# Kernel optimization log

Hardware: AMD Instinct MI355X
Metric: run time of the kernel (lower is better)

## Reference

```python
import jax, jax.numpy as jnp
import numpy as np

N = 50000        # nodes
E = 800000       # edges (avg degree 16)
DIN = 256        # input feature dim
D = 128          # embedding_dim
B = 8            # graphs in batch
ITERS = 2        # num_iterations


def setup_inputs() -> dict:
    key = jax.random.key(0)
    ks = jax.random.split(key, 16)
    w = lambda k, shape: jax.random.normal(k, shape, jnp.float32) * 0.05
    z = lambda n: jnp.zeros((n,), jnp.float32)
    return {
        "nodes": jax.random.normal(ks[0], (N, DIN), jnp.float32),
        "edges": jax.random.randint(ks[1], (2, E), 0, N),
        "batch": jnp.sort(jax.random.randint(ks[2], (N,), 0, B)),
        # initial encoder Linear(DIN, D)
        "W_enc": w(ks[3], (DIN, D)), "b_enc": z(D),
        # parent aggregation MLP: Linear(2D, D) -> ReLU -> Linear(D, D)
        "Wp1": w(ks[4], (2 * D, D)), "bp1": z(D),
        "Wp2": w(ks[5], (D, D)), "bp2": z(D),
        # child aggregation MLP
        "Wc1": w(ks[6], (2 * D, D)), "bc1": z(D),
        "Wc2": w(ks[7], (D, D)), "bc2": z(D),
        # final agg: Linear(3D, 2D) -> ReLU -> Linear(2D, D)
        "Wf1": w(ks[8], (3 * D, 2 * D)), "bf1": z(2 * D),
        "Wf2": w(ks[9], (2 * D, D)), "bf2": z(D),
        # Conv1d(D, 2D, kernel=1) == Linear(D, 2D)
        "Wconv": w(ks[10], (D, 2 * D)), "bconv": z(2 * D),
    }


def _edge_agg(x, idx_i, idx_j, W1, b1, W2, b2, inv_deg):
    # message: mlp(cat(x_i, x_j)); scatter-sum at idx_i; degree-normalize.
    h = jnp.concatenate([x[idx_i], x[idx_j]], axis=1)         # [E, 2D]
    m = jax.nn.relu(h @ W1 + b1) @ W2 + b2                    # [E, D]
    agg = jax.ops.segment_sum(m, idx_i, num_segments=x.shape[0])
    return agg * inv_deg[:, None]


def reference(nodes, edges, batch, W_enc, b_enc, Wp1, bp1, Wp2, bp2,
              Wc1, bc1, Wc2, bc2, Wf1, bf1, Wf2, bf2, Wconv, bconv):
    src, dst = edges[0], edges[1]
    ones_e = jnp.ones((edges.shape[1],), nodes.dtype)
    deg_dst = jax.ops.segment_sum(ones_e, dst, num_segments=N)
    deg_src = jax.ops.segment_sum(ones_e, src, num_segments=N)
    inv_dst = jnp.where(deg_dst > 0, 1.0 / deg_dst, 0.0)
    inv_src = jnp.where(deg_src > 0, 1.0 / deg_src, 0.0)

    x = nodes @ W_enc + b_enc                                  # [N, D]
    for _ in range(ITERS):
        # Parent_Aggregation: x_i = x[dst], x_j = x[src], sum at dst, / in-deg
        fi = _edge_agg(x, dst, src, Wp1, bp1, Wp2, bp2, inv_dst)
        # Child_Aggregation:  x_i = x[src], x_j = x[dst], sum at src, / out-deg
        fo = _edge_agg(x, src, dst, Wc1, bc1, Wc2, bc2, inv_src)
        h = jnp.concatenate([x, fi, fo], axis=1)               # [N, 3D]
        x = x + (jax.nn.relu(h @ Wf1 + bf1) @ Wf2 + bf2)

    y = x @ Wconv + bconv                                      # conv1d k=1 -> [N, 2D]
    gmax = jax.ops.segment_max(y, batch, num_segments=B)       # global_max_pool
    cnt = jax.ops.segment_sum(jnp.ones((N,), y.dtype), batch, num_segments=B)
    gmean = jax.ops.segment_sum(y, batch, num_segments=B) / cnt[:, None]
    return jnp.concatenate([gmax, gmean], axis=1)              # [B, 4D]
```

## Files before the change

### kernel.cpp

```cpp
#include <hip/hip_runtime.h>
#include <hip/hip_bf16.h>
#include <float.h>

typedef __hip_bfloat16 bf16;
typedef short short8 __attribute__((ext_vector_type(8)));
typedef short short4v __attribute__((ext_vector_type(4)));
typedef float f32x4 __attribute__((ext_vector_type(4)));

__device__ __forceinline__ float toF(bf16 v) { return __bfloat162float(v); }
__device__ __forceinline__ float s2f(short s) {
    return __uint_as_float(((unsigned int)(unsigned short)s) << 16);
}
__device__ __forceinline__ short f2s(float f) {
    bf16 h = __float2bfloat16(f);
    return *(short*)&h;
}

__global__ void diag_kernel(float* __restrict__ out, float v, int n) {
    int i = blockIdx.x * 256 + threadIdx.x;
    if (i < n) out[i] = v;
}

__global__ void init_kernel(int* __restrict__ deg2, float* __restrict__ cnt_gsum,
                            float* __restrict__ gmax, int* __restrict__ flag, int n2) {
    int i = blockIdx.x * 256 + threadIdx.x;
    if (i < n2) deg2[i] = 0;
    if (i < 8 + 2048) cnt_gsum[i] = 0.f;
    if (i < 2048) gmax[i] = -FLT_MAX;
    if (i == 0) *flag = 1;
}

__global__ void probe_kernel(const unsigned int* __restrict__ w, int nwords,
                             int* __restrict__ flag) {
    int i = blockIdx.x * 256 + threadIdx.x;
    bool bad = false;
    if (i < nwords) {
        float v = __uint_as_float((w[i] & 0xFFFFu) << 16);
        bad = !(v > -1e3f && v < 1e3f);
    }
    if (__any(bad) && (threadIdx.x & 63) == 0) atomicAnd(flag, 0);
}

struct M1 {
    const int* edges; int E; int CAP;
    int* degd; int* degs; int* adjd; int* adjs;
    const void* nsrc; bf16* ndst; int nElems;
    const void* bsrc[8]; bf16* bdst[8]; int bn[8];
    const void* wsrc[10]; int woff[10]; bf16* wdst[10];
    int wK[10]; int wNC[10]; int wstart[11];
    const int* batch; int Nn; float* cnt;
    const int* flag;
    int sCnt, sSwz, sBias, sConv;
};

__global__ void mega1_kernel(M1 a) {
    int b = blockIdx.x, tid = threadIdx.x;
    if (b < a.sCnt) {
        const int* es = a.edges;
        const int* ed = a.edges + a.E;
        int e0 = (b * 256 + tid) * 4;
        if (e0 + 4 <= a.E) {
            int4 s4 = *(const int4*)(es + e0);
            int4 d4 = *(const int4*)(ed + e0);
            int sl;
            sl = atomicAdd(&a.degs[s4.x], 1); a.adjs[s4.x * a.CAP + sl] = d4.x;
            sl = atomicAdd(&a.degs[s4.y], 1); a.adjs[s4.y * a.CAP + sl] = d4.y;
            sl = atomicAdd(&a.degs[s4.z], 1); a.adjs[s4.z * a.CAP + sl] = d4.z;
            sl = atomicAdd(&a.degs[s4.w], 1); a.adjs[s4.w * a.CAP + sl] = d4.w;
            sl = atomicAdd(&a.degd[d4.x], 1); a.adjd[d4.x * a.CAP + sl] = s4.x;
            sl = atomicAdd(&a.degd[d4.y], 1); a.adjd[d4.y * a.CAP + sl] = s4.y;
            sl = atomicAdd(&a.degd[d4.z], 1); a.adjd[d4.z * a.CAP + sl] = s4.z;
            sl = atomicAdd(&a.degd[d4.w], 1); a.adjd[d4.w * a.CAP + sl] = s4.w;
        } else {
            for (int e = e0; e < a.E; ++e) {
                int s_ = es[e], d_ = ed[e];
                int sl = atomicAdd(&a.degs[s_], 1); a.adjs[s_ * a.CAP + sl] = d_;
                sl     = atomicAdd(&a.degd[d_], 1); a.adjd[d_ * a.CAP + sl] = s_;
            }
        }
    } else if (b < a.sSwz) {
        __shared__ float loc[8];
        if (tid < 8) loc[tid] = 0.f;
        __syncthreads();
        int i = (b - a.sCnt) * 256 + tid;
        if (i < a.Nn) atomicAdd(&loc[a.batch[i]], 1.0f);
        __syncthreads();
        if (tid < 8 && loc[tid] > 0.f) atomicAdd(&a.cnt[tid], loc[tid]);
    } else if (b < a.sBias) {
        int bb = b - a.sSwz;
        int seg = 0;
#pragma unroll
        for (int t = 1; t < 10; ++t) if (bb >= a.wstart[t]) seg = t;
        int i = (bb - a.wstart[seg]) * 256 + tid;
        int K = a.wK[seg], NC = a.wNC[seg];
        if (i < K * NC) {
            int KF = K >> 5;
            int j = i & 7;
            int ln = (i >> 3) & 63;
            int q = i >> 9;
            int kb = q % KF;
            int t = q / KF;
            int k = kb * 32 + (ln >> 4) * 8 + j;
            int n = t * 16 + (ln & 15);
            int idx = a.woff[seg] + k * NC + n;
            a.wdst[seg][i] = (*a.flag)
                ? ((const bf16*)a.wsrc[seg])[idx]
                : __float2bfloat16(((const float*)a.wsrc[seg])[idx]);
        }
    } else if (b < a.sConv) {
#pragma unroll
        for (int t = 0; t < 8; ++t)
            for (int i = tid; i < a.bn[t]; i += 256)
                a.bdst[t][i] = (*a.flag)
                    ? ((const bf16*)a.bsrc[t])[i]
                    : __float2bfloat16(((const float*)a.bsrc[t])[i]);
    } else {
        if (*a.flag) return;
        int i = (b - a.sConv) * 2048 + tid * 8;
        if (i + 8 <= a.nElems) {
            const float* f = (const float*)a.nsrc + i;
            short8 o;
#pragma unroll
            for (int j = 0; j < 8; ++j) o[j] = f2s(f[j]);
            *(short8*)((short*)a.ndst + i) = o;
        } else {
            int e = a.nElems;
            for (int jj = i; jj < e && jj < i + 8; ++jj)
                a.ndst[jj] = __float2bfloat16(((const float*)a.nsrc)[jj]);
        }
    }
}

__device__ __forceinline__ void atomicMaxF(float* addr, float val) {
    unsigned int* ua = (unsigned int*)addr;
    unsigned int old = __float_as_uint(*addr);
    while (__uint_as_float(old) < val) {
        unsigned int assumed = old;
        old = atomicCAS(ua, assumed, __float_as_uint(val));
        if (old == assumed) break;
    }
}

template<int K, int NC> struct SB {
    static constexpr int APAD = K + 8;
    static constexpr int CPAD = NC + 8;
    static constexpr int AB = 64 * APAD * 2;
    static constexpr int CB = 64 * CPAD * 2;
    static constexpr int S = AB > CB ? AB : CB;
};

template<int K, int NC, int NSRC, bool RELU, bool RES, bool SCALE, bool POOL, bool STORE>
__device__ __forceinline__ void gemm_core(int bx,
    const bf16* A0, const bf16* A1, const bf16* A2,
    const bf16* WS, const bf16* bias, const float* scale, bf16* C, int M,
    const int* batch, float* gmax, float* gsum, char* smem) {
    constexpr int KF = K / 32;
    constexpr int NH = NC / 128;
    constexpr int APAD = SB<K, NC>::APAD;
    constexpr int CPAD = SB<K, NC>::CPAD;
    short* sA = (short*)smem;

    int tid = threadIdx.x;
    int m0blk = bx * 64;

    constexpr int C8 = K / 8;
    for (int idx = tid; idx < 64 * C8; idx += 256) {
        int r = idx / C8, c8 = idx % C8;
        int row = m0blk + r; row = row < M ? row : M - 1;
        const bf16* src;
        int off;
        if (NSRC == 1) { src = A0; off = c8 * 8; }
        else {
            int seg = c8 >> 4;
            src = seg == 0 ? A0 : (seg == 1 ? A1 : A2);
            off = (c8 & 15) * 8;
        }
        const size_t rs = (NSRC == 1) ? (size_t)K : (size_t)128;
        *(short8*)(sA + r * APAD + c8 * 8) = *(const short8*)((const short*)src + (size_t)row * rs + off);
    }
    __syncthreads();

    int wv = tid >> 6, ln = tid & 63;
    int quad = ln >> 4, ncol = ln & 15;
    int mw = wv * 16;

    short8 a[KF];
#pragma unroll
    for (int kb = 0; kb < KF; ++kb)
        a[kb] = *(const short8*)(sA + (mw + ncol) * APAD + kb * 32 + quad * 8);
    __syncthreads();

    float scl[4];
    if (SCALE) {
#pragma unroll
        for (int r = 0; r < 4; ++r) {
            int orow = m0blk + mw + quad * 4 + r;
            scl[r] = scale[orow < M ? orow : M - 1];
        }
    }

    short* sC = (short*)smem;
    const short8* wsp = (const short8*)WS;
#pragma unroll
    for (int h = 0; h < NH; ++h) {
        f32x4 acc[8];
#pragma unroll
        for (int t = 0; t < 8; ++t) acc[t] = (f32x4){0.f, 0.f, 0.f, 0.f};
        short8 bcur[8], bnxt[8];
#pragma unroll
        for (int t = 0; t < 8; ++t)
            bcur[t] = wsp[(size_t)((h * 8 + t) * KF) * 64 + ln];
#pragma unroll
        for (int kb = 0; kb < KF; ++kb) {
            if (kb + 1 < KF) {
#pragma unroll
                for (int t = 0; t < 8; ++t)
                    bnxt[t] = wsp[(size_t)((h * 8 + t) * KF + kb + 1) * 64 + ln];
            }
#pragma unroll
            for (int t = 0; t < 8; ++t)
                acc[t] = __builtin_amdgcn_mfma_f32_16x16x32_bf16(a[kb], bcur[t], acc[t], 0, 0, 0);
#pragma unroll
            for (int t = 0; t < 8; ++t) bcur[t] = bnxt[t];
        }
#pragma unroll
        for (int t = 0; t < 8; ++t) {
            float bv = bias ? toF(bias[h * 128 + t * 16 + ncol]) : 0.f;
#pragma unroll
            for (int r = 0; r < 4; ++r) {
                float v = acc[t][r];
                if (SCALE) { v *= scl[r]; if (scl[r] > 0.f) v += bv; }
                else v += bv;
                if (RELU) v = fmaxf(v, 0.f);
                sC[(mw + quad * 4 + r) * CPAD + h * 128 + t * 16 + ncol] = f2s(v);
            }
        }
    }
    __syncthreads();
    if (!STORE && !POOL) return;

    if (POOL) {
        int* bs = (int*)(smem + SB<K, NC>::S);
        if (tid < 64) {
            int row = m0blk + tid;
            bs[tid] = (row < M) ? batch[row] : -1;
        }
        __syncthreads();
        int cur_b = -1;
        float mx = -FLT_MAX, sm = 0.f;
        for (int r = 0; r < 64; ++r) {
            int b = bs[r];
            if (b < 0) break;
            float v = s2f(sC[r * CPAD + tid]);
            if (b != cur_b) {
                if (cur_b >= 0) {
                    atomicMaxF(&gmax[cur_b * 256 + tid], mx);
                    atomicAdd(&gsum[cur_b * 256 + tid], sm);
                }
                cur_b = b; mx = v; sm = v;
            } else {
                mx = fmaxf(mx, v);
                sm += v;
            }
        }
        if (cur_b >= 0) {
            atomicMaxF(&gmax[cur_b * 256 + tid], mx);
            atomicAdd(&gsum[cur_b * 256 + tid], sm);
        }
    } else {
        constexpr int OC8 = NC / 8;
        for (int idx = tid; idx < 64 * OC8; idx += 256) {
            int r = idx / OC8, c8 = idx % OC8;
            int row = m0blk + r;
            if (row < M) {
                short8 v = *(short8*)(sC + r * CPAD + c8 * 8);
                size_t o = (size_t)row * NC + c8 * 8;
                if (RES) {
                    short8 old = *(const short8*)((const short*)C + o);
#pragma unroll
                    for (int j = 0; j < 8; ++j) v[j] = f2s(s2f(v[j]) + s2f(old[j]));
                }
                *(short8*)((short*)C + o) = v;
            }
        }
    }
}

template<int K, int NC, int NSRC, bool RELU, bool RES, bool SCALE, bool POOL>
__global__ __launch_bounds__(256, 2)
void gemm_mfma_kernel(const bf16* A0, const bf16* A1, const bf16* A2,
                      const bf16* WS, const bf16* bias,
                      const float* scale, bf16* C, int M,
                      const int* batch, float* gmax, float* gsum) {
    __shared__ __align__(16) char smem[SB<K, NC>::S + (POOL ? 256 : 0)];
    gemm_core<K, NC, NSRC, RELU, RES, SCALE, POOL, true>(
        blockIdx.x, A0, A1, A2, WS, bias, scale, C, M, batch, gmax, gsum, smem);
}

__global__ __launch_bounds__(256, 2)
void enc_inv_kernel(const void* nodes_raw, const bf16* Tn, const int* flag,
                    const bf16* WSenc, const bf16* benc, bf16* x, int M, int gb,
                    const int* degd, const int* degs,
                    float* invd, float* invs) {
    __shared__ __align__(16) char smem[SB<256, 128>::S];
    if ((int)blockIdx.x < gb) {
        const bf16* A0 = (*flag) ? (const bf16*)nodes_raw : Tn;
        gemm_core<256, 128, 1, false, false, false, false, true>(
            blockIdx.x, A0, nullptr, nullptr, WSenc, benc, nullptr, x, M,
            nullptr, nullptr, nullptr, smem);
    } else {
        int i = ((int)blockIdx.x - gb) * 256 + threadIdx.x;
        if (i < M) {
            int dd = degd[i]; invd[i] = dd > 0 ? 1.0f / (float)dd : 0.0f;
            int ds = degs[i]; invs[i] = ds > 0 ? 1.0f / (float)ds : 0.0f;
        }
    }
}

__global__ __launch_bounds__(256, 2)
void gemm_dual_kernel(const bf16* Sp, const bf16* WS2, const bf16* b2,
                      const float* inv, bf16* Fi,
                      const bf16* x, const bf16* WSpq, bf16* T,
                      int M, int split) {
    __shared__ __align__(16) char smem[SB<128, 256>::S];
    if (blockIdx.x < split)
        gemm_core<128, 128, 1, false, false, true, false, true>(
            blockIdx.x, Sp, nullptr, nullptr, WS2, b2, inv, Fi, M, nullptr, nullptr, nullptr, smem);
    else
        gemm_core<128, 256, 1, false, false, false, false, true>(
            blockIdx.x - split, x, nullptr, nullptr, WSpq, nullptr, nullptr, T, M, nullptr, nullptr, nullptr, smem);
}

__global__ __launch_bounds__(256, 2)
void fused_mlp_kernel(const bf16* x, const bf16* Fi, const bf16* Fo,
                      const bf16* WSf1, const bf16* bf1_,
                      const bf16* WSf2, const bf16* bf2_,
                      bf16* xio, int M) {
    __shared__ __align__(16) char smem[SB<384, 256>::S];
    gemm_core<384, 256, 3, true, false, false, false, false>(
        blockIdx.x, x, Fi, Fo, WSf1, bf1_, nullptr, nullptr, M,
        nullptr, nullptr, nullptr, smem);

    constexpr int HPAD = 264;
    constexpr int CPAD2 = 136;
    short* sH = (short*)smem;
    int tid = threadIdx.x;
    int wv = tid >> 6, ln = tid & 63;
    int quad = ln >> 4, ncol = ln & 15;
    int mw = wv * 16;
    int m0blk = blockIdx.x * 64;

    short8 a2[8];
#pragma unroll
    for (int kb = 0; kb < 8; ++kb)
        a2[kb] = *(const short8*)(sH + (mw + ncol) * HPAD + kb * 32 + quad * 8);
    __syncthreads();

    f32x4 acc[8];
#pragma unroll
    for (int t = 0; t < 8; ++t) acc[t] = (f32x4){0.f, 0.f, 0.f, 0.f};
    const short8* wsp = (const short8*)WSf2;
    short8 bcur[8], bnxt[8];
#pragma unroll
    for (int t = 0; t < 8; ++t) bcur[t] = wsp[(size_t)(t * 8) * 64 + ln];
#pragma unroll
    for (int kb = 0; kb < 8; ++kb) {
        if (kb + 1 < 8) {
#pragma unroll
            for (int t = 0; t < 8; ++t)
                bnxt[t] = wsp[(size_t)(t * 8 + kb + 1) * 64 + ln];
        }
#pragma unroll
        for (int t = 0; t < 8; ++t)
            acc[t] = __builtin_amdgcn_mfma_f32_16x16x32_bf16(a2[kb], bcur[t], acc[t], 0, 0, 0);
#pragma unroll
        for (int t = 0; t < 8; ++t) bcur[t] = bnxt[t];
    }
    short* sC2 = (short*)smem;
#pragma unroll
    for (int t = 0; t < 8; ++t) {
        float bv = toF(bf2_[t * 16 + ncol]);
#pragma unroll
        for (int r = 0; r < 4; ++r)
            sC2[(mw + quad * 4 + r) * CPAD2 + t * 16 + ncol] = f2s(acc[t][r] + bv);
    }
    __syncthreads();
    for (int idx = tid; idx < 64 * 16; idx += 256) {
        int r = idx >> 4, c8 = idx & 15;
        int row = m0blk + r;
        if (row < M) {
            short8 v = *(short8*)(sC2 + r * CPAD2 + c8 * 8);
            size_t o = (size_t)row * 128 + c8 * 8;
            short8 old = *(const short8*)((const short*)xio + o);
#pragma unroll
            for (int j = 0; j < 8; ++j) v[j] = f2s(s2f(v[j]) + s2f(old[j]));
            *(short8*)((short*)xio + o) = v;
        }
    }
}

__global__ void agg_kernel(const int* __restrict__ deg, const int* __restrict__ adj, int CAP,
                           const bf16* __restrict__ PQ, const bf16* __restrict__ b1,
                           bf16* __restrict__ S, int M) {
    int tid = threadIdx.x;
    int wv = tid >> 6, ln = tid & 63;
    int node = blockIdx.x * 4 + wv;
    if (node >= M) return;
    int c4 = ln & 31, half = ln >> 5;
    float p[4];
    {
        short4v pv = *(const short4v*)((const short*)PQ + (size_t)node * 256 + 4 * c4);
        short4v bv = *(const short4v*)((const short*)b1 + 4 * c4);
#pragma unroll
        for (int r = 0; r < 4; ++r) p[r] = s2f(pv[r]) + s2f(bv[r]);
    }
    float a[4] = {0.f, 0.f, 0.f, 0.f};
    int beg = node * CAP;
    int end = beg + deg[node];
    const short* Qb = (const short*)PQ + 128 + 4 * c4;
    int k = beg + half;
    for (; k + 14 < end; k += 16) {
        int j0 = adj[k],      j1 = adj[k + 2],  j2 = adj[k + 4],  j3 = adj[k + 6];
        int j4 = adj[k + 8],  j5 = adj[k + 10], j6 = adj[k + 12], j7 = adj[k + 14];
        short4v q0 = *(const short4v*)(Qb + (size_t)j0 * 256);
        short4v q1 = *(const short4v*)(Qb + (size_t)j1 * 256);
        short4v q2 = *(const short4v*)(Qb + (size_t)j2 * 256);
        short4v q3 = *(const short4v*)(Qb + (size_t)j3 * 256);
        short4v q4 = *(const short4v*)(Qb + (size_t)j4 * 256);
        short4v q5 = *(const short4v*)(Qb + (size_t)j5 * 256);
        short4v q6 = *(const short4v*)(Qb + (size_t)j6 * 256);
        short4v q7 = *(const short4v*)(Qb + (size_t)j7 * 256);
#pragma unroll
        for (int r = 0; r < 4; ++r)
            a[r] += fmaxf(p[r] + s2f(q0[r]), 0.f) + fmaxf(p[r] + s2f(q1[r]), 0.f)
                  + fmaxf(p[r] + s2f(q2[r]), 0.f) + fmaxf(p[r] + s2f(q3[r]), 0.f)
                  + fmaxf(p[r] + s2f(q4[r]), 0.f) + fmaxf(p[r] + s2f(q5[r]), 0.f)
                  + fmaxf(p[r] + s2f(q6[r]), 0.f) + fmaxf(p[r] + s2f(q7[r]), 0.f);
    }
    for (; k + 6 < end; k += 8) {
        int j0 = adj[k], j1 = adj[k + 2], j2 = adj[k + 4], j3 = adj[k + 6];
        short4v q0 = *(const short4v*)(Qb + (size_t)j0 * 256);
        short4v q1 = *(const short4v*)(Qb + (size_t)j1 * 256);
        short4v q2 = *(const short4v*)(Qb + (size_t)j2 * 256);
        short4v q3 = *(const short4v*)(Qb + (size_t)j3 * 256);
#pragma unroll
        for (int r = 0; r < 4; ++r)
            a[r] += fmaxf(p[r] + s2f(q0[r]), 0.f) + fmaxf(p[r] + s2f(q1[r]), 0.f)
                  + fmaxf(p[r] + s2f(q2[r]), 0.f) + fmaxf(p[r] + s2f(q3[r]), 0.f);
    }
    for (; k < end; k += 2) {
        int j = adj[k];
        short4v q = *(const short4v*)(Qb + (size_t)j * 256);
#pragma unroll
        for (int r = 0; r < 4; ++r) a[r] += fmaxf(p[r] + s2f(q[r]), 0.f);
    }
#pragma unroll
    for (int r = 0; r < 4; ++r) a[r] += __shfl_xor(a[r], 32);
    if (half == 0) {
        short4v o;
#pragma unroll
        for (int r = 0; r < 4; ++r) o[r] = f2s(a[r]);
        *(short4v*)((short*)S + (size_t)node * 128 + 4 * c4) = o;
    }
}

__global__ void out_kernel(const float* __restrict__ gmax, const float* __restrict__ gsum,
                           const float* __restrict__ cnt, const int* __restrict__ flag,
                           void* __restrict__ out) {
    int i = blockIdx.x * 256 + threadIdx.x;
    if (i < 8 * 512) {
        int b = i >> 9, c = i & 511;
        float v = (c < 256) ? gmax[b * 256 + c] : gsum[b * 256 + (c - 256)] / cnt[b];
        int f = *flag;
        if (!(v == v)) v = 1000.f + 100.f * (float)f;
        if (f) ((bf16*)out)[i] = __float2bfloat16(v);
        else   ((float*)out)[i] = v;
    }
}

extern "C" void kernel_launch(void* const* d_in, const int* in_sizes, int n_in,
                              void* d_out, int out_size, void* d_ws, size_t ws_size,
                              hipStream_t stream) {
    const int* edges = (const int*)d_in[1];
    const int* batch = (const int*)d_in[2];

    const int N_ = in_sizes[2];
    const int E_ = in_sizes[1] / 2;
    const size_t ND = (size_t)N_ * 128;

    char* p = (char*)d_ws;
    bf16* x  = (bf16*)p;      p += ND * 2;
    bf16* T  = (bf16*)p;      p += (size_t)N_ * 256 * 2;
    bf16* S  = (bf16*)p;      p += ND * 2;
    bf16* Fi = (bf16*)p;      p += ND * 2;
    bf16* bias[8];
    for (int t = 0; t < 8; ++t) { bias[t] = (bf16*)p; p += 512 * 2; }
    bf16* WSenc  = (bf16*)p;  p += 256 * 128 * 2;
    bf16* WSpq_p = (bf16*)p;  p += 256 * 128 * 2;
    bf16* WSpq_c = (bf16*)p;  p += 256 * 128 * 2;
    bf16* WS2p   = (bf16*)p;  p += 128 * 128 * 2;
    bf16* WS2c   = (bf16*)p;  p += 128 * 128 * 2;
    bf16* WSf1   = (bf16*)p;  p += 384 * 256 * 2;
    bf16* WSf2   = (bf16*)p;  p += 256 * 128 * 2;
    bf16* WSconv = (bf16*)p;  p += 128 * 256 * 2;
    int* degd    = (int*)p;   p += (size_t)N_ * 4;
    int* degs    = (int*)p;   p += (size_t)N_ * 4;
    float* invd  = (float*)p; p += (size_t)N_ * 4;
    float* invs  = (float*)p; p += (size_t)N_ * 4;
    float* cnt   = (float*)p; p += 8 * 4;
    float* gsum  = (float*)p; p += 2048 * 4;
    float* gmax  = (float*)p; p += 2048 * 4;
    int* flag    = (int*)p;   p += 64;

    size_t used = (size_t)(p - (char*)d_ws);
    size_t rem = ws_size > used ? ws_size - used : 0;
    int CAP = 0;
    if (rem >= (size_t)2 * N_ * 64 * 4) CAP = 64;
    else if (rem >= (size_t)2 * N_ * 48 * 4) CAP = 48;
    if (!CAP) {
        diag_kernel<<<(out_size + 255) / 256, 256, 0, stream>>>((float*)d_out, (float)(ws_size >> 20), out_size);
        return;
    }
    int* adjd = (int*)p;      p += (size_t)N_ * CAP * 4;
    int* adjs = (int*)p;

    int gN  = (N_ + 255) / 256;
    int gE4 = (E_ + 1023) / 1024;
    int gb  = (N_ + 63) / 64;
    int ga  = (N_ + 3) / 4;

    init_kernel<<<(2 * N_ + 255) / 256, 256, 0, stream>>>(degd, cnt, gmax, flag, 2 * N_);
    probe_kernel<<<8, 256, 0, stream>>>((const unsigned int*)d_in[3], 2048, flag);

    M1 a;
    a.edges = edges; a.E = E_; a.CAP = CAP;
    a.degd = degd; a.degs = degs; a.adjd = adjd; a.adjs = adjs;
    a.nsrc = d_in[0]; a.ndst = T; a.nElems = in_sizes[0];
    {
        const int bidx[8] = {4, 6, 8, 10, 12, 14, 16, 18};
        for (int t = 0; t < 8; ++t) {
            a.bsrc[t] = d_in[bidx[t]];
            a.bdst[t] = bias[t];
            a.bn[t] = in_sizes[bidx[t]];
        }
        const void* wraw[10] = {d_in[3], d_in[5], d_in[5], d_in[9], d_in[9],
                                d_in[7], d_in[11], d_in[13], d_in[15], d_in[17]};
        int woff[10]  = {0, 0, 128 * 128, 0, 128 * 128, 0, 0, 0, 0, 0};
        bf16* wdst[10] = {WSenc, WSpq_p, WSpq_p + 128 * 128, WSpq_c, WSpq_c + 128 * 128,
                          WS2p, WS2c, WSf1, WSf2, WSconv};
        int wK[10]  = {256, 128, 128, 128, 128, 128, 128, 384, 256, 128};
        int wNC[10] = {128, 128, 128, 128, 128, 128, 128, 256, 128, 256};
        int wb_ = 0;
        for (int t = 0; t < 10; ++t) {
            a.wsrc[t] = wraw[t]; a.woff[t] = woff[t]; a.wdst[t] = wdst[t];
            a.wK[t] = wK[t]; a.wNC[t] = wNC[t];
            a.wstart[t] = wb_;
            wb_ += (wK[t] * wNC[t] + 255) / 256;
        }
        a.wstart[10] = wb_;
        a.batch = batch; a.Nn = N_; a.cnt = cnt; a.flag = flag;
        a.sCnt  = gE4;
        a.sSwz  = a.sCnt + gN;
        a.sBias = a.sSwz + wb_;
        a.sConv = a.sBias + 1;
        int convB = (a.nElems + 2047) / 2048;
        mega1_kernel<<<a.sConv + convB, 256, 0, stream>>>(a);
    }

    enc_inv_kernel<<<gb + gN, 256, 0, stream>>>(d_in[0], T, flag, WSenc, bias[0],
                                                x, N_, gb, degd, degs, invd, invs);

    for (int it = 0; it < 2; ++it) {
        gemm_mfma_kernel<128, 256, 1, false, false, false, false><<<gb, 256, 0, stream>>>(
            x, nullptr, nullptr, WSpq_p, nullptr, nullptr, T, N_, nullptr, nullptr, nullptr);
        agg_kernel<<<ga, 256, 0, stream>>>(degd, adjd, CAP, T, bias[1], S, N_);
        gemm_dual_kernel<<<2 * gb, 256, 0, stream>>>(S, WS2p, bias[2], invd, Fi,
                                                     x, WSpq_c, T, N_, gb);
        agg_kernel<<<ga, 256, 0, stream>>>(degs, adjs, CAP, T, bias[3], S, N_);
        gemm_mfma_kernel<128, 128, 1, false, false, true, false><<<gb, 256, 0, stream>>>(
            S, nullptr, nullptr, WS2c, bias[4], invs, S, N_, nullptr, nullptr, nullptr);
        fused_mlp_kernel<<<gb, 256, 0, stream>>>(x, Fi, S, WSf1, bias[5], WSf2, bias[6], x, N_);
    }

    gemm_mfma_kernel<128, 256, 1, false, false, false, true><<<gb, 256, 0, stream>>>(
        x, nullptr, nullptr, WSconv, bias[7], nullptr, nullptr, N_, batch, gmax, gsum);
    out_kernel<<<16, 256, 0, stream>>>(gmax, gsum, cnt, flag, d_out);
}
```

Measured before the change: 645.0 us.

## Fuse per-iteration MLPs and conv pooling, compact adjacency to u16 ranks

Edge adjacency construction is split into a rank-recording atomic pass followed by a scatter pass, and neighbour indices are stored as u16 to halve adjacency bandwidth. The parent and child projections are computed in one wide GEMM, and both aggregations run in a single launch. The second-layer GEMMs, final MLP and (on the last iteration) conv plus pooling are fused into one mega kernel, which cuts launches and round trips of intermediates through global memory. Rank is stored as u8 and N must be below 65536, which limits generality. The fused kernel uses more shared memory and registers, which may reduce occupancy.

```diff
diff --git a/kernel.cpp b/kernel.cpp
--- a/kernel.cpp
+++ b/kernel.cpp
@@ -6,6 +6,8 @@
 typedef short short8 __attribute__((ext_vector_type(8)));
 typedef short short4v __attribute__((ext_vector_type(4)));
 typedef float f32x4 __attribute__((ext_vector_type(4)));
+typedef unsigned short u16;
+typedef unsigned char u8;
 
 __device__ __forceinline__ float toF(bf16 v) { return __bfloat162float(v); }
 __device__ __forceinline__ float s2f(short s) {
@@ -42,13 +44,13 @@
 }
 
 struct M1 {
-    const int* edges; int E; int CAP;
-    int* degd; int* degs; int* adjd; int* adjs;
-    const void* nsrc; bf16* ndst; int nElems;
-    const void* bsrc[8]; bf16* bdst[8]; int bn[8];
+    const int* edges; int E;
+    int* degd; int* degs; u8* rankd; u8* ranks;
+    const int* batch; int Nn; float* cnt;
     const void* wsrc[10]; int woff[10]; bf16* wdst[10];
     int wK[10]; int wNC[10]; int wstart[11];
-    const int* batch; int Nn; float* cnt;
+    const void* bsrc[8]; bf16* bdst[8]; int bn[8];
+    const void* nsrc; bf16* ndst; int nElems;
     const int* flag;
     int sCnt, sSwz, sBias, sConv;
 };
@@ -62,20 +64,21 @@
         if (e0 + 4 <= a.E) {
             int4 s4 = *(const int4*)(es + e0);
             int4 d4 = *(const int4*)(ed + e0);
-            int sl;
-            sl = atomicAdd(&a.degs[s4.x], 1); a.adjs[s4.x * a.CAP + sl] = d4.x;
-            sl = atomicAdd(&a.degs[s4.y], 1); a.adjs[s4.y * a.CAP + sl] = d4.y;
-            sl = atomicAdd(&a.degs[s4.z], 1); a.adjs[s4.z * a.CAP + sl] = d4.z;
-            sl = atomicAdd(&a.degs[s4.w], 1); a.adjs[s4.w * a.CAP + sl] = d4.w;
-            sl = atomicAdd(&a.degd[d4.x], 1); a.adjd[d4.x * a.CAP + sl] = s4.x;
-            sl = atomicAdd(&a.degd[d4.y], 1); a.adjd[d4.y * a.CAP + sl] = s4.y;
-            sl = atomicAdd(&a.degd[d4.z], 1); a.adjd[d4.z * a.CAP + sl] = s4.z;
-            sl = atomicAdd(&a.degd[d4.w], 1); a.adjd[d4.w * a.CAP + sl] = s4.w;
+            uchar4 rs, rd;
+            rs.x = (u8)atomicAdd(&a.degs[s4.x], 1);
+            rs.y = (u8)atomicAdd(&a.degs[s4.y], 1);
+            rs.z = (u8)atomicAdd(&a.degs[s4.z], 1);
+            rs.w = (u8)atomicAdd(&a.degs[s4.w], 1);
+            rd.x = (u8)atomicAdd(&a.degd[d4.x], 1);
+            rd.y = (u8)atomicAdd(&a.degd[d4.y], 1);
+            rd.z = (u8)atomicAdd(&a.degd[d4.z], 1);
+            rd.w = (u8)atomicAdd(&a.degd[d4.w], 1);
+            *(uchar4*)(a.ranks + e0) = rs;
+            *(uchar4*)(a.rankd + e0) = rd;
         } else {
             for (int e = e0; e < a.E; ++e) {
-                int s_ = es[e], d_ = ed[e];
-                int sl = atomicAdd(&a.degs[s_], 1); a.adjs[s_ * a.CAP + sl] = d_;
-                sl     = atomicAdd(&a.degd[d_], 1); a.adjd[d_ * a.CAP + sl] = s_;
+                a.ranks[e] = (u8)atomicAdd(&a.degs[es[e]], 1);
+                a.rankd[e] = (u8)atomicAdd(&a.degd[ed[e]], 1);
             }
         }
     } else if (b < a.sSwz) {
@@ -298,18 +301,44 @@
 }
 
 __global__ __launch_bounds__(256, 2)
-void enc_inv_kernel(const void* nodes_raw, const bf16* Tn, const int* flag,
-                    const bf16* WSenc, const bf16* benc, bf16* x, int M, int gb,
-                    const int* degd, const int* degs,
-                    float* invd, float* invs) {
+void sei_kernel(const int* __restrict__ edges, int E,
+                const u8* __restrict__ rankd, const u8* __restrict__ ranks,
+                u16* __restrict__ adjd, u16* __restrict__ adjs, int CAP,
+                const void* nodes_raw, const bf16* Tn, const int* flag,
+                const bf16* WSenc, const bf16* benc, bf16* x, int M,
+                const int* degd, const int* degs,
+                float* invd, float* invs, int gsc, int gb) {
     __shared__ __align__(16) char smem[SB<256, 128>::S];
-    if ((int)blockIdx.x < gb) {
+    int b = blockIdx.x, tid = threadIdx.x;
+    if (b < gsc) {
+        int e0 = (b * 256 + tid) * 4;
+        if (e0 + 4 <= E) {
+            int4 s4 = *(const int4*)(edges + e0);
+            int4 d4 = *(const int4*)(edges + E + e0);
+            uchar4 rs = *(const uchar4*)(ranks + e0);
+            uchar4 rd = *(const uchar4*)(rankd + e0);
+            if (rs.x < CAP) adjs[s4.x * CAP + rs.x] = (u16)d4.x;
+            if (rs.y < CAP) adjs[s4.y * CAP + rs.y] = (u16)d4.y;
+            if (rs.z < CAP) adjs[s4.z * CAP + rs.z] = (u16)d4.z;
+            if (rs.w < CAP) adjs[s4.w * CAP + rs.w] = (u16)d4.w;
+            if (rd.x < CAP) adjd[d4.x * CAP + rd.x] = (u16)s4.x;
+            if (rd.y < CAP) adjd[d4.y * CAP + rd.y] = (u16)s4.y;
+            if (rd.z < CAP) adjd[d4.z * CAP + rd.z] = (u16)s4.z;
+            if (rd.w < CAP) adjd[d4.w * CAP + rd.w] = (u16)s4.w;
+        } else {
+            for (int e = e0; e < E; ++e) {
+                int s_ = edges[e], d_ = edges[E + e];
+                if (ranks[e] < CAP) adjs[s_ * CAP + ranks[e]] = (u16)d_;
+                if (rankd[e] < CAP) adjd[d_ * CAP + rankd[e]] = (u16)s_;
+            }
+        }
+    } else if (b < gsc + gb) {
         const bf16* A0 = (*flag) ? (const bf16*)nodes_raw : Tn;
         gemm_core<256, 128, 1, false, false, false, false, true>(
-            blockIdx.x, A0, nullptr, nullptr, WSenc, benc, nullptr, x, M,
+            b - gsc, A0, nullptr, nullptr, WSenc, benc, nullptr, x, M,
             nullptr, nullptr, nullptr, smem);
     } else {
-        int i = ((int)blockIdx.x - gb) * 256 + threadIdx.x;
+        int i = (b - gsc - gb) * 256 + tid;
         if (i < M) {
             int dd = degd[i]; invd[i] = dd > 0 ? 1.0f / (float)dd : 0.0f;
             int ds = degs[i]; invs[i] = ds > 0 ? 1.0f / (float)ds : 0.0f;
@@ -317,119 +346,35 @@
     }
 }
 
-__global__ __launch_bounds__(256, 2)
-void gemm_dual_kernel(const bf16* Sp, const bf16* WS2, const bf16* b2,
-                      const float* inv, bf16* Fi,
-                      const bf16* x, const bf16* WSpq, bf16* T,
-                      int M, int split) {
-    __shared__ __align__(16) char smem[SB<128, 256>::S];
-    if (blockIdx.x < split)
-        gemm_core<128, 128, 1, false, false, true, false, true>(
-            blockIdx.x, Sp, nullptr, nullptr, WS2, b2, inv, Fi, M, nullptr, nullptr, nullptr, smem);
-    else
-        gemm_core<128, 256, 1, false, false, false, false, true>(
-            blockIdx.x - split, x, nullptr, nullptr, WSpq, nullptr, nullptr, T, M, nullptr, nullptr, nullptr, smem);
-}
-
-__global__ __launch_bounds__(256, 2)
-void fused_mlp_kernel(const bf16* x, const bf16* Fi, const bf16* Fo,
-                      const bf16* WSf1, const bf16* bf1_,
-                      const bf16* WSf2, const bf16* bf2_,
-                      bf16* xio, int M) {
-    __shared__ __align__(16) char smem[SB<384, 256>::S];
-    gemm_core<384, 256, 3, true, false, false, false, false>(
-        blockIdx.x, x, Fi, Fo, WSf1, bf1_, nullptr, nullptr, M,
-        nullptr, nullptr, nullptr, smem);
-
-    constexpr int HPAD = 264;
-    constexpr int CPAD2 = 136;
-    short* sH = (short*)smem;
-    int tid = threadIdx.x;
-    int wv = tid >> 6, ln = tid & 63;
-    int quad = ln >> 4, ncol = ln & 15;
-    int mw = wv * 16;
-    int m0blk = blockIdx.x * 64;
-
-    short8 a2[8];
-#pragma unroll
-    for (int kb = 0; kb < 8; ++kb)
-        a2[kb] = *(const short8*)(sH + (mw + ncol) * HPAD + kb * 32 + quad * 8);
-    __syncthreads();
-
-    f32x4 acc[8];
-#pragma unroll
-    for (int t = 0; t < 8; ++t) acc[t] = (f32x4){0.f, 0.f, 0.f, 0.f};
-    const short8* wsp = (const short8*)WSf2;
-    short8 bcur[8], bnxt[8];
-#pragma unroll
-    for (int t = 0; t < 8; ++t) bcur[t] = wsp[(size_t)(t * 8) * 64 + ln];
-#pragma unroll
-    for (int kb = 0; kb < 8; ++kb) {
-        if (kb + 1 < 8) {
-#pragma unroll
-            for (int t = 0; t < 8; ++t)
-                bnxt[t] = wsp[(size_t)(t * 8 + kb + 1) * 64 + ln];
-        }
-#pragma unroll
-        for (int t = 0; t < 8; ++t)
-            acc[t] = __builtin_amdgcn_mfma_f32_16x16x32_bf16(a2[kb], bcur[t], acc[t], 0, 0, 0);
-#pragma unroll
-        for (int t = 0; t < 8; ++t) bcur[t] = bnxt[t];
-    }
-    short* sC2 = (short*)smem;
-#pragma unroll
-    for (int t = 0; t < 8; ++t) {
-        float bv = toF(bf2_[t * 16 + ncol]);
-#pragma unroll
-        for (int r = 0; r < 4; ++r)
-            sC2[(mw + quad * 4 + r) * CPAD2 + t * 16 + ncol] = f2s(acc[t][r] + bv);
-    }
-    __syncthreads();
-    for (int idx = tid; idx < 64 * 16; idx += 256) {
-        int r = idx >> 4, c8 = idx & 15;
-        int row = m0blk + r;
-        if (row < M) {
-            short8 v = *(short8*)(sC2 + r * CPAD2 + c8 * 8);
-            size_t o = (size_t)row * 128 + c8 * 8;
-            short8 old = *(const short8*)((const short*)xio + o);
-#pragma unroll
-            for (int j = 0; j < 8; ++j) v[j] = f2s(s2f(v[j]) + s2f(old[j]));
-            *(short8*)((short*)xio + o) = v;
-        }
-    }
-}
-
-__global__ void agg_kernel(const int* __restrict__ deg, const int* __restrict__ adj, int CAP,
-                           const bf16* __restrict__ PQ, const bf16* __restrict__ b1,
-                           bf16* __restrict__ S, int M) {
-    int tid = threadIdx.x;
-    int wv = tid >> 6, ln = tid & 63;
-    int node = blockIdx.x * 4 + wv;
-    if (node >= M) return;
+__device__ __forceinline__ void agg_body(int node, int tid,
+        const int* __restrict__ deg, const u16* __restrict__ adj, int CAP,
+        const short* __restrict__ PQ, int stride,
+        const short* __restrict__ b1, bf16* __restrict__ S) {
+    int ln = tid & 63;
     int c4 = ln & 31, half = ln >> 5;
     float p[4];
     {
-        short4v pv = *(const short4v*)((const short*)PQ + (size_t)node * 256 + 4 * c4);
-        short4v bv = *(const short4v*)((const short*)b1 + 4 * c4);
+        short4v pv = *(const short4v*)(PQ + (size_t)node * stride + 4 * c4);
+        short4v bv = *(const short4v*)(b1 + 4 * c4);
 #pragma unroll
         for (int r = 0; r < 4; ++r) p[r] = s2f(pv[r]) + s2f(bv[r]);
     }
     float a[4] = {0.f, 0.f, 0.f, 0.f};
-    int beg = node * CAP;
-    int end = beg + deg[node];
-    const short* Qb = (const short*)PQ + 128 + 4 * c4;
-    int k = beg + half;
-    for (; k + 14 < end; k += 16) {
-        int j0 = adj[k],      j1 = adj[k + 2],  j2 = adj[k + 4],  j3 = adj[k + 6];
-        int j4 = adj[k + 8],  j5 = adj[k + 10], j6 = adj[k + 12], j7 = adj[k + 14];
-        short4v q0 = *(const short4v*)(Qb + (size_t)j0 * 256);
-        short4v q1 = *(const short4v*)(Qb + (size_t)j1 * 256);
-        short4v q2 = *(const short4v*)(Qb + (size_t)j2 * 256);
-        short4v q3 = *(const short4v*)(Qb + (size_t)j3 * 256);
-        short4v q4 = *(const short4v*)(Qb + (size_t)j4 * 256);
-        short4v q5 = *(const short4v*)(Qb + (size_t)j5 * 256);
-        short4v q6 = *(const short4v*)(Qb + (size_t)j6 * 256);
-        short4v q7 = *(const short4v*)(Qb + (size_t)j7 * 256);
+    int d = deg[node]; d = d < CAP ? d : CAP;
+    const u16* ap = adj + (size_t)node * CAP;
+    const short* Qb = PQ + 128 + 4 * c4;
+    int k = half;
+    for (; k + 14 < d; k += 16) {
+        int j0 = ap[k],      j1 = ap[k + 2],  j2 = ap[k + 4],  j3 = ap[k + 6];
+        int j4 = ap[k + 8],  j5 = ap[k + 10], j6 = ap[k + 12], j7 = ap[k + 14];
+        short4v q0 = *(const short4v*)(Qb + (size_t)j0 * stride);
+        short4v q1 = *(const short4v*)(Qb + (size_t)j1 * stride);
+        short4v q2 = *(const short4v*)(Qb + (size_t)j2 * stride);
+        short4v q3 = *(const short4v*)(Qb + (size_t)j3 * stride);
+        short4v q4 = *(const short4v*)(Qb + (size_t)j4 * stride);
+        short4v q5 = *(const short4v*)(Qb + (size_t)j5 * stride);
+        short4v q6 = *(const short4v*)(Qb + (size_t)j6 * stride);
+        short4v q7 = *(const short4v*)(Qb + (size_t)j7 * stride);
 #pragma unroll
         for (int r = 0; r < 4; ++r)
             a[r] += fmaxf(p[r] + s2f(q0[r]), 0.f) + fmaxf(p[r] + s2f(q1[r]), 0.f)
@@ -437,20 +382,20 @@
                   + fmaxf(p[r] + s2f(q4[r]), 0.f) + fmaxf(p[r] + s2f(q5[r]), 0.f)
                   + fmaxf(p[r] + s2f(q6[r]), 0.f) + fmaxf(p[r] + s2f(q7[r]), 0.f);
     }
-    for (; k + 6 < end; k += 8) {
-        int j0 = adj[k], j1 = adj[k + 2], j2 = adj[k + 4], j3 = adj[k + 6];
-        short4v q0 = *(const short4v*)(Qb + (size_t)j0 * 256);
-        short4v q1 = *(const short4v*)(Qb + (size_t)j1 * 256);
-        short4v q2 = *(const short4v*)(Qb + (size_t)j2 * 256);
-        short4v q3 = *(const short4v*)(Qb + (size_t)j3 * 256);
+    for (; k + 6 < d; k += 8) {
+        int j0 = ap[k], j1 = ap[k + 2], j2 = ap[k + 4], j3 = ap[k + 6];
+        short4v q0 = *(const short4v*)(Qb + (size_t)j0 * stride);
+        short4v q1 = *(const short4v*)(Qb + (size_t)j1 * stride);
+        short4v q2 = *(const short4v*)(Qb + (size_t)j2 * stride);
+        short4v q3 = *(const short4v*)(Qb + (size_t)j3 * stride);
 #pragma unroll
         for (int r = 0; r < 4; ++r)
             a[r] += fmaxf(p[r] + s2f(q0[r]), 0.f) + fmaxf(p[r] + s2f(q1[r]), 0.f)
                   + fmaxf(p[r] + s2f(q2[r]), 0.f) + fmaxf(p[r] + s2f(q3[r]), 0.f);
     }
-    for (; k < end; k += 2) {
-        int j = adj[k];
-        short4v q = *(const short4v*)(Qb + (size_t)j * 256);
+    for (; k < d; k += 2) {
+        int j = ap[k];
+        short4v q = *(const short4v*)(Qb + (size_t)j * stride);
 #pragma unroll
         for (int r = 0; r < 4; ++r) a[r] += fmaxf(p[r] + s2f(q[r]), 0.f);
     }
@@ -461,6 +406,233 @@
 #pragma unroll
         for (int r = 0; r < 4; ++r) o[r] = f2s(a[r]);
         *(short4v*)((short*)S + (size_t)node * 128 + 4 * c4) = o;
+    }
+}
+
+__global__ void agg_kernel(const int* deg, const u16* adj, int CAP,
+                           const bf16* PQ, int stride, const bf16* b1,
+                           bf16* S, int M) {
+    int node = blockIdx.x * 4 + (threadIdx.x >> 6);
+    if (node >= M) return;
+    agg_body(node, threadIdx.x, deg, adj, CAP, (const short*)PQ, stride,
+             (const short*)b1, S);
+}
+
+__global__ void agg2_kernel(const int* degd, const u16* adjd,
+                            const int* degs, const u16* adjs, int CAP,
+                            const bf16* T, const bf16* b1p, const bf16* b1c,
+                            bf16* Sd, bf16* Ss, int M, int ga) {
+    int b = blockIdx.x, wv = threadIdx.x >> 6;
+    if (b < ga) {
+        int node = b * 4 + wv;
+        if (node < M)
+            agg_body(node, threadIdx.x, degd, adjd, CAP, (const short*)T, 512,
+                     (const short*)b1p, Sd);
+    } else {
+        int node = (b - ga) * 4 + wv;
+        if (node < M)
+            agg_body(node, threadIdx.x, degs, adjs, CAP, (const short*)T + 256, 512,
+                     (const short*)b1c, Ss);
+    }
+}
+
+template<bool FINAL>
+__global__ __launch_bounds__(256, 2)
+void mega_mlp_kernel(const bf16* __restrict__ x, const bf16* Sd, const bf16* Ss,
+                     const bf16* WS2p, const bf16* b2p, const float* invd,
+                     const bf16* WS2c, const bf16* b2c, const float* invs,
+                     const bf16* WSf1, const bf16* bf1_,
+                     const bf16* WSf2, const bf16* bf2_,
+                     bf16* xio, int M,
+                     const bf16* WSconv, const bf16* bconv,
+                     const int* batch, float* gmax, float* gsum) {
+    __shared__ __align__(16) char smem[52224 + 256];
+    constexpr int RB = 17408;
+    short* sm = (short*)smem;
+    int tid = threadIdx.x;
+    int m0blk = blockIdx.x * 64;
+
+    for (int idx = tid; idx < 64 * 16; idx += 256) {
+        int r = idx >> 4, c8 = idx & 15;
+        int row = m0blk + r; row = row < M ? row : M - 1;
+        *(short8*)(sm + r * 136 + c8 * 8) =
+            *(const short8*)((const short*)x + (size_t)row * 128 + c8 * 8);
+    }
+    gemm_core<128, 128, 1, false, false, true, false, false>(
+        blockIdx.x, Sd, nullptr, nullptr, WS2p, b2p, invd, nullptr, M,
+        nullptr, nullptr, nullptr, smem + RB);
+    gemm_core<128, 128, 1, false, false, true, false, false>(
+        blockIdx.x, Ss, nullptr, nullptr, WS2c, b2c, invs, nullptr, M,
+        nullptr, nullptr, nullptr, smem + 2 * RB);
+
+    int wv = tid >> 6, ln = tid & 63;
+    int quad = ln >> 4, ncol = ln & 15;
+    int mw = wv * 16;
+
+    short8 a1[12];
+#pragma unroll
+    for (int kb = 0; kb < 12; ++kb) {
+        const short* sb = sm + (kb >> 2) * (RB / 2);
+        a1[kb] = *(const short8*)(sb + (mw + ncol) * 136 + (kb & 3) * 32 + quad * 8);
+    }
+    __syncthreads();
+
+    short* sH = sm + RB / 2;
+    const short8* w1 = (const short8*)WSf1;
+#pragma unroll
+    for (int h = 0; h < 2; ++h) {
+        f32x4 acc[8];
+#pragma unroll
+        for (int t = 0; t < 8; ++t) acc[t] = (f32x4){0.f, 0.f, 0.f, 0.f};
+        short8 bcur[8], bnxt[8];
+#pragma unroll
+        for (int t = 0; t < 8; ++t)
+            bcur[t] = w1[(size_t)((h * 8 + t) * 12) * 64 + ln];
+#pragma unroll
+        for (int kb = 0; kb < 12; ++kb) {
+            if (kb + 1 < 12) {
+#pragma unroll
+                for (int t = 0; t < 8; ++t)
+                    bnxt[t] = w1[(size_t)((h * 8 + t) * 12 + kb + 1) * 64 + ln];
+            }
+#pragma unroll
+            for (int t = 0; t < 8; ++t)
+                acc[t] = __builtin_amdgcn_mfma_f32_16x16x32_bf16(a1[kb], bcur[t], acc[t], 0, 0, 0);
+#pragma unroll
+            for (int t = 0; t < 8; ++t) bcur[t] = bnxt[t];
+        }
+#pragma unroll
+        for (int t = 0; t < 8; ++t) {
+            float bv = toF(bf1_[h * 128 + t * 16 + ncol]);
+#pragma unroll
+            for (int r = 0; r < 4; ++r)
+                sH[(mw + quad * 4 + r) * 264 + h * 128 + t * 16 + ncol] =
+                    f2s(fmaxf(acc[t][r] + bv, 0.f));
+        }
+    }
+    __syncthreads();
+
+    short8 a2[8];
+#pragma unroll
+    for (int kb = 0; kb < 8; ++kb)
+        a2[kb] = *(const short8*)(sH + (mw + ncol) * 264 + kb * 32 + quad * 8);
+    __syncthreads();
+
+    f32x4 acc2[8];
+#pragma unroll
+    for (int t = 0; t < 8; ++t) acc2[t] = (f32x4){0.f, 0.f, 0.f, 0.f};
+    const short8* w2 = (const short8*)WSf2;
+    {
+        short8 bcur[8], bnxt[8];
+#pragma unroll
+        for (int t = 0; t < 8; ++t) bcur[t] = w2[(size_t)(t * 8) * 64 + ln];
+#pragma unroll
+        for (int kb = 0; kb < 8; ++kb) {
+            if (kb + 1 < 8) {
+#pragma unroll
+                for (int t = 0; t < 8; ++t)
+                    bnxt[t] = w2[(size_t)(t * 8 + kb + 1) * 64 + ln];
+            }
+#pragma unroll
+            for (int t = 0; t < 8; ++t)
+                acc2[t] = __builtin_amdgcn_mfma_f32_16x16x32_bf16(a2[kb], bcur[t], acc2[t], 0, 0, 0);
+#pragma unroll
+            for (int t = 0; t < 8; ++t) bcur[t] = bnxt[t];
+        }
+    }
+    short* sC2 = sm + RB / 2;
+#pragma unroll
+    for (int t = 0; t < 8; ++t) {
+        float bv = toF(bf2_[t * 16 + ncol]);
+#pragma unroll
+        for (int r = 0; r < 4; ++r)
+            sC2[(mw + quad * 4 + r) * 136 + t * 16 + ncol] = f2s(acc2[t][r] + bv);
+    }
+    __syncthreads();
+
+    for (int idx = tid; idx < 64 * 16; idx += 256) {
+        int r = idx >> 4, c8 = idx & 15;
+        short8 v = *(short8*)(sC2 + r * 136 + c8 * 8);
+        short8 old = *(const short8*)(sm + r * 136 + c8 * 8);
+#pragma unroll
+        for (int j = 0; j < 8; ++j) v[j] = f2s(s2f(v[j]) + s2f(old[j]));
+        if (FINAL) {
+            *(short8*)(sC2 + r * 136 + c8 * 8) = v;
+        } else {
+            int row = m0blk + r;
+            if (row < M) *(short8*)((short*)xio + (size_t)row * 128 + c8 * 8) = v;
+        }
+    }
+    if (!FINAL) return;
+    __syncthreads();
+
+    short8 a3[4];
+#pragma unroll
+    for (int kb = 0; kb < 4; ++kb)
+        a3[kb] = *(const short8*)(sC2 + (mw + ncol) * 136 + kb * 32 + quad * 8);
+    __syncthreads();
+
+    short* sCc = sm;
+    const short8* wc = (const short8*)WSconv;
+#pragma unroll
+    for (int h = 0; h < 2; ++h) {
+        f32x4 acc[8];
+#pragma unroll
+        for (int t = 0; t < 8; ++t) acc[t] = (f32x4){0.f, 0.f, 0.f, 0.f};
+        short8 bcur[8], bnxt[8];
+#pragma unroll
+        for (int t = 0; t < 8; ++t)
+            bcur[t] = wc[(size_t)((h * 8 + t) * 4) * 64 + ln];
+#pragma unroll
+        for (int kb = 0; kb < 4; ++kb) {
+            if (kb + 1 < 4) {
+#pragma unroll
+                for (int t = 0; t < 8; ++t)
+                    bnxt[t] = wc[(size_t)((h * 8 + t) * 4 + kb + 1) * 64 + ln];
+            }
+#pragma unroll
+            for (int t = 0; t < 8; ++t)
+                acc[t] = __builtin_amdgcn_mfma_f32_16x16x32_bf16(a3[kb], bcur[t], acc[t], 0, 0, 0);
+#pragma unroll
+            for (int t = 0; t < 8; ++t) bcur[t] = bnxt[t];
+        }
+#pragma unroll
+        for (int t = 0; t < 8; ++t) {
+            float bv = toF(bconv[h * 128 + t * 16 + ncol]);
+#pragma unroll
+            for (int r = 0; r < 4; ++r)
+                sCc[(mw + quad * 4 + r) * 264 + h * 128 + t * 16 + ncol] =
+                    f2s(acc[t][r] + bv);
+        }
+    }
+    __syncthreads();
+
+    int* bs = (int*)(smem + 52224);
+    if (tid < 64) {
+        int row = m0blk + tid;
+        bs[tid] = (row < M) ? batch[row] : -1;
+    }
+    __syncthreads();
+    int cur_b = -1;
+    float mx = -FLT_MAX, sum_ = 0.f;
+    for (int r = 0; r < 64; ++r) {
+        int b = bs[r];
+        if (b < 0) break;
+        float v = s2f(sCc[r * 264 + tid]);
+        if (b != cur_b) {
+            if (cur_b >= 0) {
+                atomicMaxF(&gmax[cur_b * 256 + tid], mx);
+                atomicAdd(&gsum[cur_b * 256 + tid], sum_);
+            }
+            cur_b = b; mx = v; sum_ = v;
+        } else {
+            mx = fmaxf(mx, v);
+            sum_ += v;
+        }
+    }
+    if (cur_b >= 0) {
+        atomicMaxF(&gmax[cur_b * 256 + tid], mx);
+        atomicAdd(&gsum[cur_b * 256 + tid], sum_);
     }
 }
 
@@ -490,19 +662,17 @@
 
     char* p = (char*)d_ws;
     bf16* x  = (bf16*)p;      p += ND * 2;
-    bf16* T  = (bf16*)p;      p += (size_t)N_ * 256 * 2;
-    bf16* S  = (bf16*)p;      p += ND * 2;
-    bf16* Fi = (bf16*)p;      p += ND * 2;
+    bf16* Sd = (bf16*)p;      p += ND * 2;
+    bf16* Ss = (bf16*)p;      p += ND * 2;
     bf16* bias[8];
     for (int t = 0; t < 8; ++t) { bias[t] = (bf16*)p; p += 512 * 2; }
-    bf16* WSenc  = (bf16*)p;  p += 256 * 128 * 2;
-    bf16* WSpq_p = (bf16*)p;  p += 256 * 128 * 2;
-    bf16* WSpq_c = (bf16*)p;  p += 256 * 128 * 2;
-    bf16* WS2p   = (bf16*)p;  p += 128 * 128 * 2;
-    bf16* WS2c   = (bf16*)p;  p += 128 * 128 * 2;
-    bf16* WSf1   = (bf16*)p;  p += 384 * 256 * 2;
-    bf16* WSf2   = (bf16*)p;  p += 256 * 128 * 2;
-    bf16* WSconv = (bf16*)p;  p += 128 * 256 * 2;
+    bf16* WSenc   = (bf16*)p; p += 256 * 128 * 2;
+    bf16* WSpqall = (bf16*)p; p += 4 * 128 * 128 * 2;
+    bf16* WS2p    = (bf16*)p; p += 128 * 128 * 2;
+    bf16* WS2c    = (bf16*)p; p += 128 * 128 * 2;
+    bf16* WSf1    = (bf16*)p; p += 384 * 256 * 2;
+    bf16* WSf2    = (bf16*)p; p += 256 * 128 * 2;
+    bf16* WSconv  = (bf16*)p; p += 128 * 256 * 2;
     int* degd    = (int*)p;   p += (size_t)N_ * 4;
     int* degs    = (int*)p;   p += (size_t)N_ * 4;
     float* invd  = (float*)p; p += (size_t)N_ * 4;
@@ -511,18 +681,24 @@
     float* gsum  = (float*)p; p += 2048 * 4;
     float* gmax  = (float*)p; p += 2048 * 4;
     int* flag    = (int*)p;   p += 64;
+    u8* rankd    = (u8*)p;    p += ((size_t)E_ + 15) & ~(size_t)15;
+    u8* ranks    = (u8*)p;    p += ((size_t)E_ + 15) & ~(size_t)15;
 
     size_t used = (size_t)(p - (char*)d_ws);
     size_t rem = ws_size > used ? ws_size - used : 0;
-    int CAP = 0;
-    if (rem >= (size_t)2 * N_ * 64 * 4) CAP = 64;
-    else if (rem >= (size_t)2 * N_ * 48 * 4) CAP = 48;
+    int CAP = 0, wide = 0;
+    if (N_ < 65536) {
+        if      (rem >= (size_t)2 * N_ * 64 * 2 + (size_t)N_ * 512 * 2) { CAP = 64; wide = 1; }
+        else if (rem >= (size_t)2 * N_ * 64 * 2 + (size_t)N_ * 256 * 2) { CAP = 64; wide = 0; }
+        else if (rem >= (size_t)2 * N_ * 48 * 2 + (size_t)N_ * 256 * 2) { CAP = 48; wide = 0; }
+    }
     if (!CAP) {
         diag_kernel<<<(out_size + 255) / 256, 256, 0, stream>>>((float*)d_out, (float)(ws_size >> 20), out_size);
         return;
     }
-    int* adjd = (int*)p;      p += (size_t)N_ * CAP * 4;
-    int* adjs = (int*)p;
+    u16* adjd = (u16*)p;      p += (size_t)N_ * CAP * 2;
+    u16* adjs = (u16*)p;      p += (size_t)N_ * CAP * 2;
+    bf16* T   = (bf16*)p;
 
     int gN  = (N_ + 255) / 256;
     int gE4 = (E_ + 1023) / 1024;
@@ -533,8 +709,9 @@
     probe_kernel<<<8, 256, 0, stream>>>((const unsigned int*)d_in[3], 2048, flag);
 
     M1 a;
-    a.edges = edges; a.E = E_; a.CAP = CAP;
-    a.degd = degd; a.degs = degs; a.adjd = adjd; a.adjs = adjs;
+    a.edges = edges; a.E = E_;
+    a.degd = degd; a.degs = degs; a.rankd = rankd; a.ranks = ranks;
+    a.batch = batch; a.Nn = N_; a.cnt = cnt;
     a.nsrc = d_in[0]; a.ndst = T; a.nElems = in_sizes[0];
     {
         const int bidx[8] = {4, 6, 8, 10, 12, 14, 16, 18};
@@ -546,7 +723,7 @@
         const void* wraw[10] = {d_in[3], d_in[5], d_in[5], d_in[9], d_in[9],
                                 d_in[7], d_in[11], d_in[13], d_in[15], d_in[17]};
         int woff[10]  = {0, 0, 128 * 128, 0, 128 * 128, 0, 0, 0, 0, 0};
-        bf16* wdst[10] = {WSenc, WSpq_p, WSpq_p + 128 * 128, WSpq_c, WSpq_c + 128 * 128,
+        bf16* wdst[10] = {WSenc, WSpqall, WSpqall + 16384, WSpqall + 32768, WSpqall + 49152,
                           WS2p, WS2c, WSf1, WSf2, WSconv};
         int wK[10]  = {256, 128, 128, 128, 128, 128, 128, 384, 256, 128};
         int wNC[10] = {128, 128, 128, 128, 128, 128, 128, 256, 128, 256};
@@ -558,7 +735,7 @@
             wb_ += (wK[t] * wNC[t] + 255) / 256;
         }
         a.wstart[10] = wb_;
-        a.batch = batch; a.Nn = N_; a.cnt = cnt; a.flag = flag;
+        a.flag = flag;
         a.sCnt  = gE4;
         a.sSwz  = a.sCnt + gN;
         a.sBias = a.sSwz + wb_;
@@ -567,22 +744,36 @@
         mega1_kernel<<<a.sConv + convB, 256, 0, stream>>>(a);
     }
 
-    enc_inv_kernel<<<gb + gN, 256, 0, stream>>>(d_in[0], T, flag, WSenc, bias[0],
-                                                x, N_, gb, degd, degs, invd, invs);
+    sei_kernel<<<gE4 + gb + gN, 256, 0, stream>>>(
+        edges, E_, rankd, ranks, adjd, adjs, CAP,
+        d_in[0], T, flag, WSenc, bias[0], x, N_,
+        degd, degs, invd, invs, gE4, gb);
 
     for (int it = 0; it < 2; ++it) {
-        gemm_mfma_kernel<128, 256, 1, false, false, false, false><<<gb, 256, 0, stream>>>(
-            x, nullptr, nullptr, WSpq_p, nullptr, nullptr, T, N_, nullptr, nullptr, nullptr);
-        agg_kernel<<<ga, 256, 0, stream>>>(degd, adjd, CAP, T, bias[1], S, N_);
-        gemm_dual_kernel<<<2 * gb, 256, 0, stream>>>(S, WS2p, bias[2], invd, Fi,
-                                                     x, WSpq_c, T, N_, gb);
-        agg_kernel<<<ga, 256, 0, stream>>>(degs, adjs, CAP, T, bias[3], S, N_);
-        gemm_mfma_kernel<128, 128, 1, false, false, true, false><<<gb, 256, 0, stream>>>(
-            S, nullptr, nullptr, WS2c, bias[4], invs, S, N_, nullptr, nullptr, nullptr);
-        fused_mlp_kernel<<<gb, 256, 0, stream>>>(x, Fi, S, WSf1, bias[5], WSf2, bias[6], x, N_);
-    }
-
-    gemm_mfma_kernel<128, 256, 1, false, false, false, true><<<gb, 256, 0, stream>>>(
-        x, nullptr, nullptr, WSconv, bias[7], nullptr, nullptr, N_, batch, gmax, gsum);
+        if (wide) {
+            gemm_mfma_kernel<128, 512, 1, false, false, false, false><<<gb, 256, 0, stream>>>(
+                x, nullptr, nullptr, WSpqall, nullptr, nullptr, T, N_, nullptr, nullptr, nullptr);
+            agg2_kernel<<<2 * ga, 256, 0, stream>>>(degd, adjd, degs, adjs, CAP,
+                                                    T, bias[1], bias[3], Sd, Ss, N_, ga);
+        } else {
+            gemm_mfma_kernel<128, 256, 1, false, false, false, false><<<gb, 256, 0, stream>>>(
+                x, nullptr, nullptr, WSpqall, nullptr, nullptr, T, N_, nullptr, nullptr, nullptr);
+            agg_kernel<<<ga, 256, 0, stream>>>(degd, adjd, CAP, T, 256, bias[1], Sd, N_);
+            gemm_mfma_kernel<128, 256, 1, false, false, false, false><<<gb, 256, 0, stream>>>(
+                x, nullptr, nullptr, WSpqall + 32768, nullptr, nullptr, T, N_, nullptr, nullptr, nullptr);
+            agg_kernel<<<ga, 256, 0, stream>>>(degs, adjs, CAP, T, 256, bias[3], Ss, N_);
+        }
+        if (it == 0)
+            mega_mlp_kernel<false><<<gb, 256, 0, stream>>>(
+                x, Sd, Ss, WS2p, bias[2], invd, WS2c, bias[4], invs,
+                WSf1, bias[5], WSf2, bias[6], x, N_,
+                WSconv, bias[7], batch, gmax, gsum);
+        else
+            mega_mlp_kernel<true><<<gb, 256, 0, stream>>>(
+                x, Sd, Ss, WS2p, bias[2], invd, WS2c, bias[4], invs,
+                WSf1, bias[5], WSf2, bias[6], x, N_,
+                WSconv, bias[7], batch, gmax, gsum);
+    }
+
     out_kernel<<<16, 256, 0, stream>>>(gmax, gsum, cnt, flag, d_out);
 }
```

After: 626.9 us. 2.8% less time.
